# Optimization experiments

Measured on AMD Instinct MI355X. Metric: run time of the kernel, lower is better.

## Reference

```python
import jax, jax.numpy as jnp
import numpy as np

N = 100_000
E = 1_600_000
IN, HID, OUT, ED = 128, 128, 64, 16
NEG_SLOPE = 0.2  # PyG GATConv default leaky_relu slope


def segment_softmax(logits, seg, num_segments):
    m = jax.ops.segment_max(logits, seg, num_segments=num_segments)
    m = jnp.where(jnp.isfinite(m), m, 0.0)
    e = jnp.exp(logits - m[seg])
    s = jax.ops.segment_sum(e, seg, num_segments=num_segments)
    return e / (s[seg] + 1e-16)


def gat_conv(x, edge_index, W, a_src, a_dst, b, edge_attr=None, We=None, ae=None):
    """PyG GATConv, heads=1, add_self_loops=True, fill_value='mean'."""
    n = x.shape[0]
    h = x @ W  # [N, C]
    loop = jnp.arange(n, dtype=edge_index.dtype)
    src = jnp.concatenate([edge_index[0], loop])  # [E+N]
    dst = jnp.concatenate([edge_index[1], loop])
    alpha = (h * a_src).sum(-1)[src] + (h * a_dst).sum(-1)[dst]  # [E+N]
    if edge_attr is not None:
        # self-loop edge_attr filled with per-destination mean (PyG fill_value='mean')
        cnt = jax.ops.segment_sum(jnp.ones((edge_attr.shape[0],), edge_attr.dtype), edge_index[1], num_segments=n)
        mean_attr = jax.ops.segment_sum(edge_attr, edge_index[1], num_segments=n) / jnp.maximum(cnt, 1.0)[:, None]
        ea = jnp.concatenate([edge_attr, mean_attr], axis=0)  # [E+N, ED]
        alpha = alpha + (ea @ We) @ ae
    alpha = jax.nn.leaky_relu(alpha, NEG_SLOPE)
    alpha = segment_softmax(alpha, dst, n)
    out = jax.ops.segment_sum(alpha[:, None] * h[src], dst, num_segments=n)  # scatter-add
    return out + b


def setup_inputs() -> dict:
    key = jax.random.key(0)
    ks = iter(jax.random.split(key, 32))
    g = lambda shape, fan: (jax.random.normal(next(ks), shape, jnp.float32) * (1.0 / np.sqrt(fan)))
    inp = {
        "x": jax.random.normal(next(ks), (N, IN), jnp.float32),
        "edge_index": jax.random.randint(next(ks), (2, E), 0, N, jnp.int32),
        "edge_attr": jax.random.normal(next(ks), (E, ED), jnp.float32),
        # conv1 (no edge_attr)
        "W1": g((IN, HID), IN), "a1_src": g((HID,), HID), "a1_dst": g((HID,), HID), "b1": jnp.zeros((HID,), jnp.float32),
        # conv2 (with edge_attr)
        "W2": g((HID, HID), HID), "a2_src": g((HID,), HID), "a2_dst": g((HID,), HID), "b2": jnp.zeros((HID,), jnp.float32),
        "We2": g((ED, HID), ED), "ae2": g((HID,), HID),
        # initial residual linear
        "Wr": g((IN, HID), IN), "br": jnp.zeros((HID,), jnp.float32),
        # conv_mu
        "Wmu": g((HID, OUT), HID), "amu_src": g((OUT,), OUT), "amu_dst": g((OUT,), OUT), "bmu": jnp.zeros((OUT,), jnp.float32),
        "Wemu": g((ED, OUT), ED), "aemu": g((OUT,), OUT),
        # conv_logstd
        "Wls": g((HID, OUT), HID), "als_src": g((OUT,), OUT), "als_dst": g((OUT,), OUT), "bls": jnp.zeros((OUT,), jnp.float32),
        "Wels": g((ED, OUT), ED), "aels": g((OUT,), OUT),
    }
    return inp


def reference(x, edge_index, edge_attr,
              W1, a1_src, a1_dst, b1,
              W2, a2_src, a2_dst, b2, We2, ae2,
              Wr, br,
              Wmu, amu_src, amu_dst, bmu, Wemu, aemu,
              Wls, als_src, als_dst, bls, Wels, aels):
    h = jax.nn.relu(gat_conv(x, edge_index, W1, a1_src, a1_dst, b1))
    h = jax.nn.relu(gat_conv(h, edge_index, W2, a2_src, a2_dst, b2, edge_attr, We2, ae2))
    h = h + (x @ Wr + br)  # initial residual
    mu = gat_conv(h, edge_index, Wmu, amu_src, amu_dst, bmu, edge_attr, Wemu, aemu)
    logstd = gat_conv(h, edge_index, Wls, als_src, als_dst, bls, edge_attr, Wels, aels)
    return mu, logstd
```

## Files before the change

### kernel.cpp

```cpp
#include <hip/hip_runtime.h>

#define NN 100000
#define NE 1600000
#define BSH 9
#define NBUK 196
#define NPG 8

typedef __attribute__((ext_vector_type(8))) short bf16x8;
typedef __attribute__((ext_vector_type(4))) float f32x4;

__device__ __forceinline__ float grp_sum16(float v){
  #pragma unroll
  for (int o = 8; o; o >>= 1) v += __shfl_xor(v, o, 16);
  return v;
}
__device__ __forceinline__ float grp_sum32(float v){
  #pragma unroll
  for (int o = 16; o; o >>= 1) v += __shfl_xor(v, o, 32);
  return v;
}
__device__ __forceinline__ float bf2f(unsigned short x){
  return __uint_as_float(((unsigned)x) << 16);
}
__device__ __forceinline__ unsigned short f2bf(float f){
  unsigned u = __float_as_uint(f);
  return (unsigned short)((u + 0x7FFFu + ((u >> 16) & 1u)) >> 16);
}

__global__ void prep_w_kernel(const float* __restrict__ W1, const float* __restrict__ W2,
                              const float* __restrict__ Wr, const float* __restrict__ Wmu,
                              const float* __restrict__ Wls,
                              unsigned short* __restrict__ W1t, unsigned short* __restrict__ W2t,
                              unsigned short* __restrict__ Wrt, unsigned short* __restrict__ Wmlt){
  int b = blockIdx.x, t = threadIdx.x;
  for (int it = 0; it < 64; it++){
    int idx = it*256 + t;
    int k = idx >> 7, c = idx & 127;
    float v; unsigned short* dst;
    if (b == 0){ v = W1[k*128+c]; dst = W1t; }
    else if (b == 1){ v = W2[k*128+c]; dst = W2t; }
    else if (b == 2){ v = Wr[k*128+c]; dst = Wrt; }
    else { v = (c & 1) ? Wls[k*64 + (c>>1)] : Wmu[k*64 + (c>>1)]; dst = Wmlt; }
    dst[c*128 + k] = f2bf(v);
  }
}

__global__ void wvec_kernel(const float* __restrict__ We2, const float* __restrict__ ae2,
                            const float* __restrict__ Wemu, const float* __restrict__ aemu,
                            const float* __restrict__ Wels, const float* __restrict__ aels,
                            float* __restrict__ wv){
  int t = threadIdx.x;
  if (t < 16){
    float s = 0.f; for (int c = 0; c < 128; c++) s += We2[t*128+c]*ae2[c];
    wv[t] = s;
  } else if (t < 32){
    int k = t-16; float s = 0.f; for (int c = 0; c < 64; c++) s += Wemu[k*64+c]*aemu[c];
    wv[16+k] = s;
  } else if (t < 48){
    int k = t-32; float s = 0.f; for (int c = 0; c < 64; c++) s += Wels[k*64+c]*aels[c];
// ... 94 lines not shown
    hbase[t] = c ? atomicAdd(&gbfill[t], c) : 0u;
  }
  __syncthreads();
  #pragma unroll
  for (int k = 0; k < 4; k++){
    if (val[k]){
      unsigned pos = atomicAdd(&hcur[b[k]], 1);
      unsigned slot = gbbase[b[k]] + hbase[b[k]] + pos;
      bdu[slot] = make_uint2((unsigned)d[k], (unsigned)u[k]);
      bw[slot]  = w[k];
    }
  }
}

__global__ __launch_bounds__(1024) void place_kernel(const uint2* __restrict__ bdu,
                                                     const float4* __restrict__ bw,
                                                     const unsigned* __restrict__ gbbase,
                                                     int* __restrict__ rowptr,
                                                     unsigned* __restrict__ csr_u,
                                                     float* __restrict__ ewp2,
                                                     float2* __restrict__ ewpmuls){
  __shared__ unsigned h[512], incl[512], cur[512];
  int b = blockIdx.x, t = threadIdx.x;
  unsigned cbase = gbbase[b];
  unsigned cnt = gbbase[b+1] - cbase;
  if (t < 512) h[t] = 0;
  __syncthreads();
  for (unsigned i = t; i < cnt; i += 1024)
    atomicAdd(&h[bdu[cbase+i].x & 511], 1);
  __syncthreads();
  if (t < 512) incl[t] = h[t];
  __syncthreads();
  for (int o = 1; o < 512; o <<= 1){
    unsigned add = (t >= o && t < 512) ? incl[t-o] : 0;
    __syncthreads();
    if (t < 512) incl[t] += add;
    __syncthreads();
  }
  if (t < 512){
    cur[t] = 0;
    int node = (b << BSH) + t;
    if (node < NN) rowptr[node] = (int)(cbase + incl[t] - h[t]);
  }
  __syncthreads();
  for (unsigned i = t; i < cnt; i += 1024){
    uint2 du = bdu[cbase+i];
    unsigned ld = du.x & 511;
    unsigned pos = atomicAdd(&cur[ld], 1);
    unsigned slot = cbase + (incl[ld] - h[ld]) + pos;
    float4 w = bw[cbase+i];
    csr_u[slot] = du.y;
    ewp2[slot] = w.x;
    ewpmuls[slot] = make_float2(w.y, w.z);
  }
}

template<int OUT, int DOTS>
__global__ __launch_bounds__(256) void gemm_bf16(const unsigned short* __restrict__ Xb,
                                                 const unsigned short* __restrict__ Wt,
                                                 void* __restrict__ Y,
                                                 const float* __restrict__ bias, int nrows,
                                                 const float* __restrict__ va,
                                                 const float* __restrict__ vb,
                                                 const float* __restrict__ vc,
                                                 const float* __restrict__ vd,
                                                 float* __restrict__ sOut,
                                                 float* __restrict__ dOut){
  __shared__ uint4 As[128*16];
  __shared__ uint4 Bs[128*16];
  int t = threadIdx.x;
  int row0 = blockIdx.x * 128;
  #pragma unroll
  for (int p = 0; p < 8; p++){
    int idx = p*256 + t;
    int r = idx >> 4, cir = idx & 15;
    uint4 v = make_uint4(0,0,0,0);
    if (row0 + r < nrows) v = *(const uint4*)(Xb + ((size_t)(row0+r))*128 + cir*8);
    As[r*16 + (cir ^ (r & 7))] = v;
  }
  #pragma unroll
  for (int p = 0; p < 8; p++){
    int idx = p*256 + t;
    int r = idx >> 4, cir = idx & 15;
    Bs[r*16 + (cir ^ (r & 7))] = *(const uint4*)(Wt + (size_t)r*128 + cir*8);
  }
  __syncthreads();
  int w = t >> 6, l = t & 63;
  int lr = l & 15;
  int lk = l >> 4;
  const bf16x8* As8 = (const bf16x8*)As;
  const bf16x8* Bs8 = (const bf16x8*)Bs;
  f32x4 acc[2][8];
  f32x4 zero = {0.f, 0.f, 0.f, 0.f};
  #pragma unroll
  for (int m = 0; m < 2; m++)
    #pragma unroll
    for (int n = 0; n < 8; n++) acc[m][n] = zero;
  #pragma unroll
  for (int ks = 0; ks < 4; ks++){
    bf16x8 a0, a1, bf[8];
    { int r = w*32 + lr;      a0 = As8[r*16 + ((ks*4+lk) ^ (r&7))]; }
    { int r = w*32 + 16 + lr; a1 = As8[r*16 + ((ks*4+lk) ^ (r&7))]; }
    #pragma unroll
    for (int nt = 0; nt < 8; nt++){
      int r = nt*16 + lr;
      bf[nt] = Bs8[r*16 + ((ks*4+lk) ^ (r&7))];
// ... 24 lines not shown
    }
  }
  if constexpr (DOTS == 2){
    #pragma unroll
    for (int mt = 0; mt < 2; mt++){
      #pragma unroll
      for (int i = 0; i < 4; i++){
        float pmu = 0.f, pdm = 0.f, pls = 0.f, pdl = 0.f;
        #pragma unroll
        for (int nt = 0; nt < 8; nt++){
          float av = acc[mt][nt][i];
          int col = nt*16 + lr;
          int c = col >> 1;
          if (col & 1){ pls = fmaf(av, vc[c], pls); pdl = fmaf(av, vd[c], pdl); }
          else        { pmu = fmaf(av, va[c], pmu); pdm = fmaf(av, vb[c], pdm); }
        }
        pmu = grp_sum16(pmu); pdm = grp_sum16(pdm);
        pls = grp_sum16(pls); pdl = grp_sum16(pdl);
        int r = row0 + w*32 + mt*16 + lk*4 + i;
        if (lr == 0 && r < nrows){
          ((float2*)sOut)[r] = make_float2(pmu, pls);
          ((float2*)dOut)[r] = make_float2(pdm, pdl);
        }
      }
    }
  }
  #pragma unroll
  for (int mt = 0; mt < 2; mt++){
    int gr0 = row0 + w*32 + mt*16 + lk*4;
    #pragma unroll
    for (int nt = 0; nt < 8; nt++){
      int col = nt*16 + lr;
      float bv = (OUT >= 1) ? bias[col] : 0.f;
      #pragma unroll
      for (int i = 0; i < 4; i++){
        int r = gr0 + i;
        if (r < nrows){
          float o = acc[mt][nt][i] + bv;
          if constexpr (OUT == 1) ((float*)Y)[(size_t)r*128 + col] = o;
          else ((unsigned short*)Y)[(size_t)r*128 + col] = f2bf(o);
        }
      }
    }
  }
}

template<bool HAS_EW>
__global__ __launch_bounds__(256) void agg_conv(const unsigned short* __restrict__ Hb,
                                                const float* __restrict__ s,
                                                const float* __restrict__ dsc,
                                                const float* __restrict__ ewp,
                                                const int* __restrict__ rowptr,
                                                const unsigned* __restrict__ csr_u,
                                                const float* __restrict__ bias,
                                                const unsigned short* __restrict__ residb,
                                                unsigned short* __restrict__ out){
  int g = (blockIdx.x * blockDim.x + threadIdx.x) >> 5;
  int lig = threadIdx.x & 31;
  int c0 = lig*4;
  float4 bv = *(const float4*)(bias + c0);
  int v0 = g * NPG;
  int vend = v0 + NPG; if (vend > NN) vend = NN;
  for (int v = v0; v < vend; v++){
    int rs = rowptr[v], re = rowptr[v+1];
    int deg = re - rs;
    float d_v = dsc[v];
    float acc[4] = {0.f,0.f,0.f,0.f};
    float pl = 0.f, ewl = 0.f;
    for (int base = rs; base < re; base += 32){
      int i = base + lig;
      int u = 0; float w = 0.f;
      if (i < re){
        u = (int)csr_u[i];
        float e = HAS_EW ? ewp[i] : 0.f;
        if (HAS_EW) ewl += e;
        float a = s[u] + d_v + e;
        float l = a > 0.f ? a : 0.2f*a;
        w = __expf(l);
      }
      pl += w;
      int nv = re - base; if (nv > 32) nv = 32;
      for (int j = 0; j < nv; j += 8){
        uint2 q[8]; float wj[8];
        #pragma unroll
        for (int k = 0; k < 8; k++){
          int uk = __shfl(u, j+k, 32);
          wj[k] = __shfl(w, j+k, 32);
          q[k] = *(const uint2*)(Hb + (size_t)uk*128 + c0);
        }
        #pragma unroll
        for (int k = 0; k < 8; k++){
          acc[0] = fmaf(wj[k], __uint_as_float(q[k].x << 16), acc[0]);
          acc[1] = fmaf(wj[k], __uint_as_float(q[k].x & 0xFFFF0000u), acc[1]);
          acc[2] = fmaf(wj[k], __uint_as_float(q[k].y << 16), acc[2]);
          acc[3] = fmaf(wj[k], __uint_as_float(q[k].y & 0xFFFF0000u), acc[3]);
        }
      }
    }
    float p = grp_sum32(pl);
    float ews = HAS_EW ? grp_sum32(ewl) : 0.f;
    float selfa = s[v] + d_v + (HAS_EW ? ews / (float)(deg > 1 ? deg : 1) : 0.f);
    float lself = selfa > 0.f ? selfa : 0.2f*selfa;
    float wself = __expf(lself);
    p += wself;
    {
      uint2 q = *(const uint2*)(Hb + (size_t)v*128 + c0);
      acc[0] = fmaf(wself, __uint_as_float(q.x << 16), acc[0]);
      acc[1] = fmaf(wself, __uint_as_float(q.x & 0xFFFF0000u), acc[1]);
      acc[2] = fmaf(wself, __uint_as_float(q.y << 16), acc[2]);
      acc[3] = fmaf(wself, __uint_as_float(q.y & 0xFFFF0000u), acc[3]);
    }
    float inv = 1.f / p;
    float o0 = fmaxf(acc[0]*inv + bv.x, 0.f);
    float o1 = fmaxf(acc[1]*inv + bv.y, 0.f);
    float o2 = fmaxf(acc[2]*inv + bv.z, 0.f);
    float o3 = fmaxf(acc[3]*inv + bv.w, 0.f);
    if (HAS_EW){
      uint2 r = *(const uint2*)(residb + (size_t)v*128 + c0);
      o0 += __uint_as_float(r.x << 16);
      o1 += __uint_as_float(r.x & 0xFFFF0000u);
      o2 += __uint_as_float(r.y << 16);
      o3 += __uint_as_float(r.y & 0xFFFF0000u);
    }
    uint2 ow;
    ow.x = (unsigned)f2bf(o0) | ((unsigned)f2bf(o1) << 16);
    ow.y = (unsigned)f2bf(o2) | ((unsigned)f2bf(o3) << 16);
    *(uint2*)(out + (size_t)v*128 + c0) = ow;
  }
}

__global__ __launch_bounds__(256) void agg_muls(const unsigned short* __restrict__ Yb,
                                                const float2* __restrict__ sg,
                                                const float2* __restrict__ dg,
                                                const float2* __restrict__ ewpmuls,
                                                const int* __restrict__ rowptr,
                                                const unsigned* __restrict__ csr_u,
                                                const float* __restrict__ bmu,
                                                const float* __restrict__ bls,
                                                float* __restrict__ outmu,
                                                float* __restrict__ outls){
  int g = (blockIdx.x * blockDim.x + threadIdx.x) >> 5;
  int lig = threadIdx.x & 31;
  int c0 = lig*2;
  float2 bmv = make_float2(bmu[c0], bmu[c0+1]);
  float2 blv = make_float2(bls[c0], bls[c0+1]);
  int v0 = g * NPG;
  int vend = v0 + NPG; if (vend > NN) vend = NN;
  for (int v = v0; v < vend; v++){
    int rs = rowptr[v], re = rowptr[v+1];
    int deg = re - rs;
    float2 dv = dg[v];
    float accmu[2] = {0.f,0.f}, accls[2] = {0.f,0.f};
    float pmu = 0.f, pls = 0.f, ewlmu = 0.f, ewlls = 0.f;
    for (int base = rs; base < re; base += 32){
      int i = base + lig;
      int u = 0; float wmu = 0.f, wls = 0.f;
      if (i < re){
        u = (int)csr_u[i];
        float2 su = sg[u];
        float2 ee = ewpmuls[i];
        ewlmu += ee.x; ewlls += ee.y;
        float amu = su.x + dv.x + ee.x;
        float als = su.y + dv.y + ee.y;
        float lmu = amu > 0.f ? amu : 0.2f*amu;
        float lls = als > 0.f ? als : 0.2f*als;
        wmu = __expf(lmu); wls = __expf(lls);
      }
      pmu += wmu; pls += wls;
      int nv = re - base; if (nv > 32) nv = 32;
      for (int j = 0; j < nv; j += 8){
        uint2 q[8]; float wm[8], wl[8];
        #pragma unroll
        for (int k = 0; k < 8; k++){
          int uk = __shfl(u, j+k, 32);
          wm[k] = __shfl(wmu, j+k, 32);
          wl[k] = __shfl(wls, j+k, 32);
          q[k] = *(const uint2*)(Yb + (size_t)uk*128 + lig*4);
        }
        #pragma unroll
        for (int k = 0; k < 8; k++){
          accmu[0] = fmaf(wm[k], __uint_as_float(q[k].x << 16), accmu[0]);
          accls[0] = fmaf(wl[k], __uint_as_float(q[k].x & 0xFFFF0000u), accls[0]);
          accmu[1] = fmaf(wm[k], __uint_as_float(q[k].y << 16), accmu[1]);
          accls[1] = fmaf(wl[k], __uint_as_float(q[k].y & 0xFFFF0000u), accls[1]);
        }
      }
    }
    float Pmu = grp_sum32(pmu), Pls = grp_sum32(pls);
    float Emu = grp_sum32(ewlmu), Els = grp_sum32(ewlls);
    float2 sv = sg[v];
    float dnm = (float)(deg > 1 ? deg : 1);
    float selfmu = sv.x + dv.x + Emu/dnm;
    float selfls = sv.y + dv.y + Els/dnm;
    float lmu = selfmu > 0.f ? selfmu : 0.2f*selfmu;
    float lls = selfls > 0.f ? selfls : 0.2f*selfls;
    float wmu_s = __expf(lmu), wls_s = __expf(lls);
    Pmu += wmu_s; Pls += wls_s;
    {
      uint2 q = *(const uint2*)(Yb + (size_t)v*128 + lig*4);
      accmu[0] = fmaf(wmu_s, __uint_as_float(q.x << 16), accmu[0]);
      accls[0] = fmaf(wls_s, __uint_as_float(q.x & 0xFFFF0000u), accls[0]);
      accmu[1] = fmaf(wmu_s, __uint_as_float(q.y << 16), accmu[1]);
      accls[1] = fmaf(wls_s, __uint_as_float(q.y & 0xFFFF0000u), accls[1]);
    }
    float imu = 1.f/Pmu, ils = 1.f/Pls;
    float2 omu = make_float2(accmu[0]*imu + bmv.x, accmu[1]*imu + bmv.y);
    float2 ols = make_float2(accls[0]*ils + blv.x, accls[1]*ils + blv.y);
    *(float2*)(outmu + (size_t)v*64 + c0) = omu;
    *(float2*)(outls + (size_t)v*64 + c0) = ols;
  }
}

extern "C" void kernel_launch(void* const* d_in, const int* in_sizes, int n_in,
                              void* d_out, int out_size, void* d_ws, size_t ws_size,
                              hipStream_t stream){
  const float* x    = (const float*)d_in[0];
  const int*   ei   = (const int*)  d_in[1];
  const float* ea   = (const float*)d_in[2];
  const float* W1   = (const float*)d_in[3];
  const float* a1s  = (const float*)d_in[4];
  const float* a1d  = (const float*)d_in[5];
  const float* b1   = (const float*)d_in[6];
  const float* W2   = (const float*)d_in[7];
  const float* a2s  = (const float*)d_in[8];
  const float* a2d  = (const float*)d_in[9];
  const float* b2   = (const float*)d_in[10];
  const float* We2  = (const float*)d_in[11];
  const float* ae2  = (const float*)d_in[12];
  const float* Wr   = (const float*)d_in[13];
  const float* br   = (const float*)d_in[14];
  const float* Wmu  = (const float*)d_in[15];
  const float* amus = (const float*)d_in[16];
  const float* amud = (const float*)d_in[17];
  const float* bmu  = (const float*)d_in[18];
  const float* Wemu = (const float*)d_in[19];
  const float* aemu = (const float*)d_in[20];
  const float* Wls  = (const float*)d_in[21];
  const float* alss = (const float*)d_in[22];
  const float* alsd = (const float*)d_in[23];
  const float* bls  = (const float*)d_in[24];
  const float* Wels = (const float*)d_in[25];
  const float* aels = (const float*)d_in[26];

  char* base = (char*)d_ws;
  size_t off = 0;
  auto alloc = [&](size_t bytes)->char*{
    char* p = base + off;
    off = (off + bytes + 511) & ~(size_t)511;
    return p;
  };
  int*      rowptr = (int*)   alloc((size_t)(NN+1)*4);
  unsigned* gbcnt  = (unsigned*)alloc(512*4);
  unsigned* gbfill = gbcnt + 256;
  unsigned* gbbase = (unsigned*)alloc(257*4);
  uint2*    bdu    = (uint2*) alloc((size_t)NE*8);
  float4*   bw     = (float4*)alloc((size_t)NE*16);
  unsigned* csr_u  = (unsigned*)alloc((size_t)NE*4);
  float*    ewp2   = (float*) alloc((size_t)NE*4);
  float2*   ewpmls = (float2*)alloc((size_t)NE*8);
  float*    wv     = (float*) alloc(48*4);
  float*    s1     = (float*) alloc((size_t)NN*4);
  float*    d1     = (float*) alloc((size_t)NN*4);
  float2*   sg2    = (float2*)alloc((size_t)NN*8);
  float2*   dg2    = (float2*)alloc((size_t)NN*8);
  unsigned short* W1t  = (unsigned short*)alloc(128*128*2);
  unsigned short* W2t  = (unsigned short*)alloc(128*128*2);
  unsigned short* Wrt  = (unsigned short*)alloc(128*128*2);
  unsigned short* Wmlt = (unsigned short*)alloc(128*128*2);
  unsigned short* Xb   = (unsigned short*)alloc((size_t)NN*128*2);
  unsigned short* XRb  = (unsigned short*)alloc((size_t)NN*128*2);
  unsigned short* bufA = (unsigned short*)alloc((size_t)NN*128*2);
  unsigned short* bufB = (unsigned short*)alloc((size_t)NN*128*2);
  if (off > ws_size) return;

  float* outF = (float*)d_out;
  float* muO  = outF;
  float* lsO  = outF + (size_t)NN*64;

  const int HB   = (NE + 4095)/4096;
  const int AGB  = ((NN + NPG - 1)/NPG * 32 + 255)/256;
  const int GB   = (NN + 127)/128;
  const int CB   = (NN*128/8 + 255)/256;

  prep_w_kernel<<<4, 256, 0, stream>>>(W1, W2, Wr, Wmu, Wls, W1t, W2t, Wrt, Wmlt);
  wvec_kernel<<<1, 64, 0, stream>>>(We2, ae2, Wemu, aemu, Wels, aels, wv);
  cast_x_kernel<<<CB, 256, 0, stream>>>(x, Xb);
  zero_kernel<<<2, 256, 0, stream>>>((int*)gbcnt, 512);
  ehist_kernel<<<HB, 1024, 0, stream>>>(ei, gbcnt);
  bscan_kernel<<<1, 256, 0, stream>>>(gbcnt, gbbase, rowptr);
  bin_kernel<<<HB, 1024, 0, stream>>>(ei, ea, wv, gbbase, gbfill, bdu, bw);
  place_kernel<<<NBUK, 1024, 0, stream>>>(bdu, bw, gbbase, rowptr, csr_u, ewp2, ewpmls);

  gemm_bf16<0,1><<<GB, 256, 0, stream>>>(Xb, W1t, bufA, nullptr, NN,
                                         a1s, a1d, nullptr, nullptr, s1, d1);
  agg_conv<false><<<AGB, 256, 0, stream>>>(bufA, s1, d1, nullptr, rowptr, csr_u,
                                           b1, nullptr, bufB);
  gemm_bf16<0,1><<<GB, 256, 0, stream>>>(bufB, W2t, bufA, nullptr, NN,
                                         a2s, a2d, nullptr, nullptr, s1, d1);
  gemm_bf16<2,0><<<GB, 256, 0, stream>>>(Xb, Wrt, XRb, br, NN,
                                         nullptr, nullptr, nullptr, nullptr,
                                         nullptr, nullptr);
  agg_conv<true><<<AGB, 256, 0, stream>>>(bufA, s1, d1, ewp2, rowptr, csr_u,
                                          b2, XRb, bufB);
  gemm_bf16<0,2><<<GB, 256, 0, stream>>>(bufB, Wmlt, bufA, nullptr, NN,
                                         amus, amud, alss, alsd,
                                         (float*)sg2, (float*)dg2);
  agg_muls<<<AGB, 256, 0, stream>>>(bufA, sg2, dg2, ewpmls, rowptr, csr_u,
                                    bmu, bls, muO, lsO);
}
```

Measured before the change: 491.6 us.

## Use persistent work-stealing groups with atomic counter in aggregation kernels

Replaces the static assignment of 8 nodes per 32-lane group with a persistent grid of 2048 blocks. Each group atomically grabs batches of 4 nodes from a global counter until all nodes are done. The goal is to balance load across groups despite varying node degrees and to cut tail imbalance. In exchange it adds one atomic per batch, which may contend on the shared counter, and per-kernel tick counters are zeroed in the setup kernel.

```diff
diff --git a/kernel.cpp b/kernel.cpp
--- a/kernel.cpp
+++ b/kernel.cpp
@@ -4,7 +4,7 @@
 #define NE 1600000
 #define BSH 9
 #define NBUK 196
-#define NPG 8
+#define TBATCH 4
 
 typedef __attribute__((ext_vector_type(8))) short bf16x8;
 typedef __attribute__((ext_vector_type(4))) float f32x4;
@@ -337,78 +337,83 @@
                                                 const unsigned* __restrict__ csr_u,
                                                 const float* __restrict__ bias,
                                                 const unsigned short* __restrict__ residb,
-                                                unsigned short* __restrict__ out){
-  int g = (blockIdx.x * blockDim.x + threadIdx.x) >> 5;
+                                                unsigned short* __restrict__ out,
+                                                unsigned* __restrict__ ctr){
   int lig = threadIdx.x & 31;
   int c0 = lig*4;
   float4 bv = *(const float4*)(bias + c0);
-  int v0 = g * NPG;
-  int vend = v0 + NPG; if (vend > NN) vend = NN;
-  for (int v = v0; v < vend; v++){
-    int rs = rowptr[v], re = rowptr[v+1];
-    int deg = re - rs;
-    float d_v = dsc[v];
-    float acc[4] = {0.f,0.f,0.f,0.f};
-    float pl = 0.f, ewl = 0.f;
-    for (int base = rs; base < re; base += 32){
-      int i = base + lig;
-      int u = 0; float w = 0.f;
-      if (i < re){
-        u = (int)csr_u[i];
-        float e = HAS_EW ? ewp[i] : 0.f;
-        if (HAS_EW) ewl += e;
-        float a = s[u] + d_v + e;
-        float l = a > 0.f ? a : 0.2f*a;
-        w = __expf(l);
-      }
-      pl += w;
-      int nv = re - base; if (nv > 32) nv = 32;
-      for (int j = 0; j < nv; j += 8){
-        uint2 q[8]; float wj[8];
-        #pragma unroll
-        for (int k = 0; k < 8; k++){
-          int uk = __shfl(u, j+k, 32);
-          wj[k] = __shfl(w, j+k, 32);
-          q[k] = *(const uint2*)(Hb + (size_t)uk*128 + c0);
-        }
-        #pragma unroll
-        for (int k = 0; k < 8; k++){
-          acc[0] = fmaf(wj[k], __uint_as_float(q[k].x << 16), acc[0]);
-          acc[1] = fmaf(wj[k], __uint_as_float(q[k].x & 0xFFFF0000u), acc[1]);
-          acc[2] = fmaf(wj[k], __uint_as_float(q[k].y << 16), acc[2]);
-          acc[3] = fmaf(wj[k], __uint_as_float(q[k].y & 0xFFFF0000u), acc[3]);
-        }
-      }
-    }
-    float p = grp_sum32(pl);
-    float ews = HAS_EW ? grp_sum32(ewl) : 0.f;
-    float selfa = s[v] + d_v + (HAS_EW ? ews / (float)(deg > 1 ? deg : 1) : 0.f);
-    float lself = selfa > 0.f ? selfa : 0.2f*selfa;
-    float wself = __expf(lself);
-    p += wself;
-    {
-      uint2 q = *(const uint2*)(Hb + (size_t)v*128 + c0);
-      acc[0] = fmaf(wself, __uint_as_float(q.x << 16), acc[0]);
-      acc[1] = fmaf(wself, __uint_as_float(q.x & 0xFFFF0000u), acc[1]);
-      acc[2] = fmaf(wself, __uint_as_float(q.y << 16), acc[2]);
-      acc[3] = fmaf(wself, __uint_as_float(q.y & 0xFFFF0000u), acc[3]);
-    }
-    float inv = 1.f / p;
-    float o0 = fmaxf(acc[0]*inv + bv.x, 0.f);
-    float o1 = fmaxf(acc[1]*inv + bv.y, 0.f);
-    float o2 = fmaxf(acc[2]*inv + bv.z, 0.f);
-    float o3 = fmaxf(acc[3]*inv + bv.w, 0.f);
-    if (HAS_EW){
-      uint2 r = *(const uint2*)(residb + (size_t)v*128 + c0);
-      o0 += __uint_as_float(r.x << 16);
-      o1 += __uint_as_float(r.x & 0xFFFF0000u);
-      o2 += __uint_as_float(r.y << 16);
-      o3 += __uint_as_float(r.y & 0xFFFF0000u);
-    }
-    uint2 ow;
-    ow.x = (unsigned)f2bf(o0) | ((unsigned)f2bf(o1) << 16);
-    ow.y = (unsigned)f2bf(o2) | ((unsigned)f2bf(o3) << 16);
-    *(uint2*)(out + (size_t)v*128 + c0) = ow;
+  for (;;){
+    unsigned nb = 0;
+    if (lig == 0) nb = atomicAdd(ctr, TBATCH);
+    nb = __shfl((int)nb, 0, 32);
+    if (nb >= NN) break;
+    int vend = nb + TBATCH; if (vend > NN) vend = NN;
+    for (int v = (int)nb; v < vend; v++){
+      int rs = rowptr[v], re = rowptr[v+1];
+      int deg = re - rs;
+      float d_v = dsc[v];
+      float acc[4] = {0.f,0.f,0.f,0.f};
+      float pl = 0.f, ewl = 0.f;
+      for (int base = rs; base < re; base += 32){
+        int i = base + lig;
+        int u = 0; float w = 0.f;
+        if (i < re){
+          u = (int)csr_u[i];
+          float e = HAS_EW ? ewp[i] : 0.f;
+          if (HAS_EW) ewl += e;
+          float a = s[u] + d_v + e;
+          float l = a > 0.f ? a : 0.2f*a;
+          w = __expf(l);
+        }
+        pl += w;
+        int nv = re - base; if (nv > 32) nv = 32;
+        for (int j = 0; j < nv; j += 8){
+          uint2 q[8]; float wj[8];
+          #pragma unroll
+          for (int k = 0; k < 8; k++){
+            int uk = __shfl(u, j+k, 32);
+            wj[k] = __shfl(w, j+k, 32);
+            q[k] = *(const uint2*)(Hb + (size_t)uk*128 + c0);
+          }
+          #pragma unroll
+          for (int k = 0; k < 8; k++){
+            acc[0] = fmaf(wj[k], __uint_as_float(q[k].x << 16), acc[0]);
+            acc[1] = fmaf(wj[k], __uint_as_float(q[k].x & 0xFFFF0000u), acc[1]);
+            acc[2] = fmaf(wj[k], __uint_as_float(q[k].y << 16), acc[2]);
+            acc[3] = fmaf(wj[k], __uint_as_float(q[k].y & 0xFFFF0000u), acc[3]);
+          }
+        }
+      }
+      float p = grp_sum32(pl);
+      float ews = HAS_EW ? grp_sum32(ewl) : 0.f;
+      float selfa = s[v] + d_v + (HAS_EW ? ews / (float)(deg > 1 ? deg : 1) : 0.f);
+      float lself = selfa > 0.f ? selfa : 0.2f*selfa;
+      float wself = __expf(lself);
+      p += wself;
+      {
+        uint2 q = *(const uint2*)(Hb + (size_t)v*128 + c0);
+        acc[0] = fmaf(wself, __uint_as_float(q.x << 16), acc[0]);
+        acc[1] = fmaf(wself, __uint_as_float(q.x & 0xFFFF0000u), acc[1]);
+        acc[2] = fmaf(wself, __uint_as_float(q.y << 16), acc[2]);
+        acc[3] = fmaf(wself, __uint_as_float(q.y & 0xFFFF0000u), acc[3]);
+      }
+      float inv = 1.f / p;
+      float o0 = fmaxf(acc[0]*inv + bv.x, 0.f);
+      float o1 = fmaxf(acc[1]*inv + bv.y, 0.f);
+      float o2 = fmaxf(acc[2]*inv + bv.z, 0.f);
+      float o3 = fmaxf(acc[3]*inv + bv.w, 0.f);
+      if (HAS_EW){
+        uint2 r = *(const uint2*)(residb + (size_t)v*128 + c0);
+        o0 += __uint_as_float(r.x << 16);
+        o1 += __uint_as_float(r.x & 0xFFFF0000u);
+        o2 += __uint_as_float(r.y << 16);
+        o3 += __uint_as_float(r.y & 0xFFFF0000u);
+      }
+      uint2 ow;
+      ow.x = (unsigned)f2bf(o0) | ((unsigned)f2bf(o1) << 16);
+      ow.y = (unsigned)f2bf(o2) | ((unsigned)f2bf(o3) << 16);
+      *(uint2*)(out + (size_t)v*128 + c0) = ow;
+    }
   }
 }
 
@@ -421,76 +426,81 @@
                                                 const float* __restrict__ bmu,
                                                 const float* __restrict__ bls,
                                                 float* __restrict__ outmu,
-                                                float* __restrict__ outls){
-  int g = (blockIdx.x * blockDim.x + threadIdx.x) >> 5;
+                                                float* __restrict__ outls,
+                                                unsigned* __restrict__ ctr){
   int lig = threadIdx.x & 31;
   int c0 = lig*2;
   float2 bmv = make_float2(bmu[c0], bmu[c0+1]);
   float2 blv = make_float2(bls[c0], bls[c0+1]);
-  int v0 = g * NPG;
-  int vend = v0 + NPG; if (vend > NN) vend = NN;
-  for (int v = v0; v < vend; v++){
-    int rs = rowptr[v], re = rowptr[v+1];
-    int deg = re - rs;
-    float2 dv = dg[v];
-    float accmu[2] = {0.f,0.f}, accls[2] = {0.f,0.f};
-    float pmu = 0.f, pls = 0.f, ewlmu = 0.f, ewlls = 0.f;
-    for (int base = rs; base < re; base += 32){
-      int i = base + lig;
-      int u = 0; float wmu = 0.f, wls = 0.f;
-      if (i < re){
-        u = (int)csr_u[i];
-        float2 su = sg[u];
-        float2 ee = ewpmuls[i];
-        ewlmu += ee.x; ewlls += ee.y;
-        float amu = su.x + dv.x + ee.x;
-        float als = su.y + dv.y + ee.y;
-        float lmu = amu > 0.f ? amu : 0.2f*amu;
-        float lls = als > 0.f ? als : 0.2f*als;
-        wmu = __expf(lmu); wls = __expf(lls);
-      }
-      pmu += wmu; pls += wls;
-      int nv = re - base; if (nv > 32) nv = 32;
-      for (int j = 0; j < nv; j += 8){
-        uint2 q[8]; float wm[8], wl[8];
-        #pragma unroll
-        for (int k = 0; k < 8; k++){
-          int uk = __shfl(u, j+k, 32);
-          wm[k] = __shfl(wmu, j+k, 32);
-          wl[k] = __shfl(wls, j+k, 32);
-          q[k] = *(const uint2*)(Yb + (size_t)uk*128 + lig*4);
-        }
-        #pragma unroll
-        for (int k = 0; k < 8; k++){
-          accmu[0] = fmaf(wm[k], __uint_as_float(q[k].x << 16), accmu[0]);
-          accls[0] = fmaf(wl[k], __uint_as_float(q[k].x & 0xFFFF0000u), accls[0]);
-          accmu[1] = fmaf(wm[k], __uint_as_float(q[k].y << 16), accmu[1]);
-          accls[1] = fmaf(wl[k], __uint_as_float(q[k].y & 0xFFFF0000u), accls[1]);
-        }
-      }
-    }
-    float Pmu = grp_sum32(pmu), Pls = grp_sum32(pls);
-    float Emu = grp_sum32(ewlmu), Els = grp_sum32(ewlls);
-    float2 sv = sg[v];
-    float dnm = (float)(deg > 1 ? deg : 1);
-    float selfmu = sv.x + dv.x + Emu/dnm;
-    float selfls = sv.y + dv.y + Els/dnm;
-    float lmu = selfmu > 0.f ? selfmu : 0.2f*selfmu;
-    float lls = selfls > 0.f ? selfls : 0.2f*selfls;
-    float wmu_s = __expf(lmu), wls_s = __expf(lls);
-    Pmu += wmu_s; Pls += wls_s;
-    {
-      uint2 q = *(const uint2*)(Yb + (size_t)v*128 + lig*4);
-      accmu[0] = fmaf(wmu_s, __uint_as_float(q.x << 16), accmu[0]);
-      accls[0] = fmaf(wls_s, __uint_as_float(q.x & 0xFFFF0000u), accls[0]);
-      accmu[1] = fmaf(wmu_s, __uint_as_float(q.y << 16), accmu[1]);
-      accls[1] = fmaf(wls_s, __uint_as_float(q.y & 0xFFFF0000u), accls[1]);
-    }
-    float imu = 1.f/Pmu, ils = 1.f/Pls;
-    float2 omu = make_float2(accmu[0]*imu + bmv.x, accmu[1]*imu + bmv.y);
-    float2 ols = make_float2(accls[0]*ils + blv.x, accls[1]*ils + blv.y);
-    *(float2*)(outmu + (size_t)v*64 + c0) = omu;
-    *(float2*)(outls + (size_t)v*64 + c0) = ols;
+  for (;;){
+    unsigned nb = 0;
+    if (lig == 0) nb = atomicAdd(ctr, TBATCH);
+    nb = __shfl((int)nb, 0, 32);
+    if (nb >= NN) break;
+    int vend = nb + TBATCH; if (vend > NN) vend = NN;
+    for (int v = (int)nb; v < vend; v++){
+      int rs = rowptr[v], re = rowptr[v+1];
+      int deg = re - rs;
+      float2 dv = dg[v];
+      float accmu[2] = {0.f,0.f}, accls[2] = {0.f,0.f};
+      float pmu = 0.f, pls = 0.f, ewlmu = 0.f, ewlls = 0.f;
+      for (int base = rs; base < re; base += 32){
+        int i = base + lig;
+        int u = 0; float wmu = 0.f, wls = 0.f;
+        if (i < re){
+          u = (int)csr_u[i];
+          float2 su = sg[u];
+          float2 ee = ewpmuls[i];
+          ewlmu += ee.x; ewlls += ee.y;
+          float amu = su.x + dv.x + ee.x;
+          float als = su.y + dv.y + ee.y;
+          float lmu = amu > 0.f ? amu : 0.2f*amu;
+          float lls = als > 0.f ? als : 0.2f*als;
+          wmu = __expf(lmu); wls = __expf(lls);
+        }
+        pmu += wmu; pls += wls;
+        int nv = re - base; if (nv > 32) nv = 32;
+        for (int j = 0; j < nv; j += 8){
+          uint2 q[8]; float wm[8], wl[8];
+          #pragma unroll
+          for (int k = 0; k < 8; k++){
+            int uk = __shfl(u, j+k, 32);
+            wm[k] = __shfl(wmu, j+k, 32);
+            wl[k] = __shfl(wls, j+k, 32);
+            q[k] = *(const uint2*)(Yb + (size_t)uk*128 + lig*4);
+          }
+          #pragma unroll
+          for (int k = 0; k < 8; k++){
+            accmu[0] = fmaf(wm[k], __uint_as_float(q[k].x << 16), accmu[0]);
+            accls[0] = fmaf(wl[k], __uint_as_float(q[k].x & 0xFFFF0000u), accls[0]);
+            accmu[1] = fmaf(wm[k], __uint_as_float(q[k].y << 16), accmu[1]);
+            accls[1] = fmaf(wl[k], __uint_as_float(q[k].y & 0xFFFF0000u), accls[1]);
+          }
+        }
+      }
+      float Pmu = grp_sum32(pmu), Pls = grp_sum32(pls);
+      float Emu = grp_sum32(ewlmu), Els = grp_sum32(ewlls);
+      float2 sv = sg[v];
+      float dnm = (float)(deg > 1 ? deg : 1);
+      float selfmu = sv.x + dv.x + Emu/dnm;
+      float selfls = sv.y + dv.y + Els/dnm;
+      float lmu = selfmu > 0.f ? selfmu : 0.2f*selfmu;
+      float lls = selfls > 0.f ? selfls : 0.2f*selfls;
+      float wmu_s = __expf(lmu), wls_s = __expf(lls);
+      Pmu += wmu_s; Pls += wls_s;
+      {
+        uint2 q = *(const uint2*)(Yb + (size_t)v*128 + lig*4);
+        accmu[0] = fmaf(wmu_s, __uint_as_float(q.x << 16), accmu[0]);
+        accls[0] = fmaf(wls_s, __uint_as_float(q.x & 0xFFFF0000u), accls[0]);
+        accmu[1] = fmaf(wmu_s, __uint_as_float(q.y << 16), accmu[1]);
+        accls[1] = fmaf(wls_s, __uint_as_float(q.y & 0xFFFF0000u), accls[1]);
+      }
+      float imu = 1.f/Pmu, ils = 1.f/Pls;
+      float2 omu = make_float2(accmu[0]*imu + bmv.x, accmu[1]*imu + bmv.y);
+      float2 ols = make_float2(accls[0]*ils + blv.x, accls[1]*ils + blv.y);
+      *(float2*)(outmu + (size_t)v*64 + c0) = omu;
+      *(float2*)(outls + (size_t)v*64 + c0) = ols;
+    }
   }
 }
 
@@ -533,8 +543,9 @@
     return p;
   };
   int*      rowptr = (int*)   alloc((size_t)(NN+1)*4);
-  unsigned* gbcnt  = (unsigned*)alloc(512*4);
+  unsigned* gbcnt  = (unsigned*)alloc(520*4);
   unsigned* gbfill = gbcnt + 256;
+  unsigned* tick   = gbcnt + 512;
   unsigned* gbbase = (unsigned*)alloc(257*4);
   uint2*    bdu    = (uint2*) alloc((size_t)NE*8);
   float4*   bw     = (float4*)alloc((size_t)NE*16);
@@ -561,14 +572,14 @@
   float* lsO  = outF + (size_t)NN*64;
 
   const int HB   = (NE + 4095)/4096;
-  const int AGB  = ((NN + NPG - 1)/NPG * 32 + 255)/256;
+  const int PGB  = 2048;
   const int GB   = (NN + 127)/128;
   const int CB   = (NN*128/8 + 255)/256;
 
   prep_w_kernel<<<4, 256, 0, stream>>>(W1, W2, Wr, Wmu, Wls, W1t, W2t, Wrt, Wmlt);
   wvec_kernel<<<1, 64, 0, stream>>>(We2, ae2, Wemu, aemu, Wels, aels, wv);
   cast_x_kernel<<<CB, 256, 0, stream>>>(x, Xb);
-  zero_kernel<<<2, 256, 0, stream>>>((int*)gbcnt, 512);
+  zero_kernel<<<3, 256, 0, stream>>>((int*)gbcnt, 520);
   ehist_kernel<<<HB, 1024, 0, stream>>>(ei, gbcnt);
   bscan_kernel<<<1, 256, 0, stream>>>(gbcnt, gbbase, rowptr);
   bin_kernel<<<HB, 1024, 0, stream>>>(ei, ea, wv, gbbase, gbfill, bdu, bw);
@@ -576,18 +587,18 @@
 
   gemm_bf16<0,1><<<GB, 256, 0, stream>>>(Xb, W1t, bufA, nullptr, NN,
                                          a1s, a1d, nullptr, nullptr, s1, d1);
-  agg_conv<false><<<AGB, 256, 0, stream>>>(bufA, s1, d1, nullptr, rowptr, csr_u,
-                                           b1, nullptr, bufB);
+  agg_conv<false><<<PGB, 256, 0, stream>>>(bufA, s1, d1, nullptr, rowptr, csr_u,
+                                           b1, nullptr, bufB, tick+0);
   gemm_bf16<0,1><<<GB, 256, 0, stream>>>(bufB, W2t, bufA, nullptr, NN,
                                          a2s, a2d, nullptr, nullptr, s1, d1);
   gemm_bf16<2,0><<<GB, 256, 0, stream>>>(Xb, Wrt, XRb, br, NN,
                                          nullptr, nullptr, nullptr, nullptr,
                                          nullptr, nullptr);
-  agg_conv<true><<<AGB, 256, 0, stream>>>(bufA, s1, d1, ewp2, rowptr, csr_u,
-                                          b2, XRb, bufB);
+  agg_conv<true><<<PGB, 256, 0, stream>>>(bufA, s1, d1, ewp2, rowptr, csr_u,
+                                          b2, XRb, bufB, tick+1);
   gemm_bf16<0,2><<<GB, 256, 0, stream>>>(bufB, Wmlt, bufA, nullptr, NN,
                                          amus, amud, alss, alsd,
                                          (float*)sg2, (float*)dg2);
-  agg_muls<<<AGB, 256, 0, stream>>>(bufA, sg2, dg2, ewpmls, rowptr, csr_u,
-                                    bmu, bls, muO, lsO);
-}
+  agg_muls<<<PGB, 256, 0, stream>>>(bufA, sg2, dg2, ewpmls, rowptr, csr_u,
+                                    bmu, bls, muO, lsO, tick+2);
+}
```

Result: slower. 1.050 ms (+113.7%).

## Sort nodes by in-degree and assign one half-wave per node in aggregation

Applied to the files above, without the earlier changes.

Adds a degree histogram, scan and scatter that build a permutation of nodes grouped by in-degree. The three aggregation kernels now map each 32-lane group to one node taken from that permutation, instead of each group looping over 8 consecutive nodes. This aims to even out work within a wavefront and raise the number of groups in flight, reducing divergence and tail imbalance from varied degrees. The cost is three extra small kernels, and output writes and neighbor reads become scattered in node order, which may reduce locality.

```diff
diff --git a/kernel.cpp b/kernel.cpp
--- a/kernel.cpp
+++ b/kernel.cpp
@@ -4,7 +4,8 @@
 #define NE 1600000
 #define BSH 9
 #define NBUK 196
-#define NPG 8
+#define NDB 64
+#define NB  ((NN + 255)/256)
 
 typedef __attribute__((ext_vector_type(8))) short bf16x8;
 typedef __attribute__((ext_vector_type(4))) float f32x4;
@@ -205,6 +206,57 @@
     csr_u[slot] = du.y;
     ewp2[slot] = w.x;
     ewpmuls[slot] = make_float2(w.y, w.z);
+  }
+}
+
+__global__ void dhist_kernel(const int* __restrict__ rowptr, unsigned* __restrict__ dcnt){
+  __shared__ unsigned h[NDB];
+  int t = threadIdx.x;
+  if (t < NDB) h[t] = 0;
+  __syncthreads();
+  int v = blockIdx.x*256 + t;
+  if (v < NN){
+    int d = rowptr[v+1] - rowptr[v]; if (d > NDB-1) d = NDB-1;
+    atomicAdd(&h[d], 1);
+  }
+  __syncthreads();
+  if (t < NDB && h[t]) atomicAdd(&dcnt[t], h[t]);
+}
+
+__global__ void dscan_kernel(const unsigned* __restrict__ dcnt, unsigned* __restrict__ dbase){
+  __shared__ unsigned sh[NDB];
+  int t = threadIdx.x;
+  unsigned v = dcnt[t];
+  sh[t] = v; __syncthreads();
+  for (int o = 1; o < NDB; o <<= 1){
+    unsigned add = (t >= o) ? sh[t-o] : 0;
+    __syncthreads();
+    sh[t] += add;
+    __syncthreads();
+  }
+  dbase[t] = sh[t] - v;
+}
+
+__global__ void dscatter_kernel(const int* __restrict__ rowptr, const unsigned* __restrict__ dbase,
+                                unsigned* __restrict__ dfill, int* __restrict__ perm){
+  __shared__ unsigned hc[NDB], hb[NDB], cur[NDB];
+  int t = threadIdx.x;
+  if (t < NDB){ hc[t] = 0; cur[t] = 0; }
+  __syncthreads();
+  int v = blockIdx.x*256 + t; int d = -1;
+  if (v < NN){
+    d = rowptr[v+1] - rowptr[v]; if (d > NDB-1) d = NDB-1;
+    atomicAdd(&hc[d], 1);
+  }
+  __syncthreads();
+  if (t < NDB){
+    unsigned c = hc[t];
+    hb[t] = c ? atomicAdd(&dfill[t], c) : 0u;
+  }
+  __syncthreads();
+  if (v < NN){
+    unsigned pos = atomicAdd(&cur[d], 1);
+    perm[dbase[d] + hb[d] + pos] = v;
   }
 }
 
@@ -335,81 +387,80 @@
                                                 const float* __restrict__ ewp,
                                                 const int* __restrict__ rowptr,
                                                 const unsigned* __restrict__ csr_u,
+                                                const int* __restrict__ perm,
                                                 const float* __restrict__ bias,
                                                 const unsigned short* __restrict__ residb,
                                                 unsigned short* __restrict__ out){
   int g = (blockIdx.x * blockDim.x + threadIdx.x) >> 5;
   int lig = threadIdx.x & 31;
+  if (g >= NN) return;
+  int v = perm[g];
+  int rs = rowptr[v], re = rowptr[v+1];
+  int deg = re - rs;
+  float d_v = dsc[v];
   int c0 = lig*4;
   float4 bv = *(const float4*)(bias + c0);
-  int v0 = g * NPG;
-  int vend = v0 + NPG; if (vend > NN) vend = NN;
-  for (int v = v0; v < vend; v++){
-    int rs = rowptr[v], re = rowptr[v+1];
-    int deg = re - rs;
-    float d_v = dsc[v];
-    float acc[4] = {0.f,0.f,0.f,0.f};
-    float pl = 0.f, ewl = 0.f;
-    for (int base = rs; base < re; base += 32){
-      int i = base + lig;
-      int u = 0; float w = 0.f;
-      if (i < re){
-        u = (int)csr_u[i];
-        float e = HAS_EW ? ewp[i] : 0.f;
-        if (HAS_EW) ewl += e;
-        float a = s[u] + d_v + e;
-        float l = a > 0.f ? a : 0.2f*a;
-        w = __expf(l);
-      }
-      pl += w;
-      int nv = re - base; if (nv > 32) nv = 32;
-      for (int j = 0; j < nv; j += 8){
-        uint2 q[8]; float wj[8];
-        #pragma unroll
-        for (int k = 0; k < 8; k++){
-          int uk = __shfl(u, j+k, 32);
-          wj[k] = __shfl(w, j+k, 32);
-          q[k] = *(const uint2*)(Hb + (size_t)uk*128 + c0);
-        }
-        #pragma unroll
-        for (int k = 0; k < 8; k++){
-          acc[0] = fmaf(wj[k], __uint_as_float(q[k].x << 16), acc[0]);
-          acc[1] = fmaf(wj[k], __uint_as_float(q[k].x & 0xFFFF0000u), acc[1]);
-          acc[2] = fmaf(wj[k], __uint_as_float(q[k].y << 16), acc[2]);
-          acc[3] = fmaf(wj[k], __uint_as_float(q[k].y & 0xFFFF0000u), acc[3]);
-        }
-      }
-    }
-    float p = grp_sum32(pl);
-    float ews = HAS_EW ? grp_sum32(ewl) : 0.f;
-    float selfa = s[v] + d_v + (HAS_EW ? ews / (float)(deg > 1 ? deg : 1) : 0.f);
-    float lself = selfa > 0.f ? selfa : 0.2f*selfa;
-    float wself = __expf(lself);
-    p += wself;
-    {
-      uint2 q = *(const uint2*)(Hb + (size_t)v*128 + c0);
-      acc[0] = fmaf(wself, __uint_as_float(q.x << 16), acc[0]);
-      acc[1] = fmaf(wself, __uint_as_float(q.x & 0xFFFF0000u), acc[1]);
-      acc[2] = fmaf(wself, __uint_as_float(q.y << 16), acc[2]);
-      acc[3] = fmaf(wself, __uint_as_float(q.y & 0xFFFF0000u), acc[3]);
-    }
-    float inv = 1.f / p;
-    float o0 = fmaxf(acc[0]*inv + bv.x, 0.f);
-    float o1 = fmaxf(acc[1]*inv + bv.y, 0.f);
-    float o2 = fmaxf(acc[2]*inv + bv.z, 0.f);
-    float o3 = fmaxf(acc[3]*inv + bv.w, 0.f);
-    if (HAS_EW){
-      uint2 r = *(const uint2*)(residb + (size_t)v*128 + c0);
-      o0 += __uint_as_float(r.x << 16);
-      o1 += __uint_as_float(r.x & 0xFFFF0000u);
-      o2 += __uint_as_float(r.y << 16);
-      o3 += __uint_as_float(r.y & 0xFFFF0000u);
-    }
-    uint2 ow;
-    ow.x = (unsigned)f2bf(o0) | ((unsigned)f2bf(o1) << 16);
-    ow.y = (unsigned)f2bf(o2) | ((unsigned)f2bf(o3) << 16);
-    *(uint2*)(out + (size_t)v*128 + c0) = ow;
-  }
+  float acc[4] = {0.f,0.f,0.f,0.f};
+  float pl = 0.f, ewl = 0.f;
+  for (int base = rs; base < re; base += 32){
+    int i = base + lig;
+    int u = 0; float w = 0.f;
+    if (i < re){
+      u = (int)csr_u[i];
+      float e = HAS_EW ? ewp[i] : 0.f;
+      if (HAS_EW) ewl += e;
+      float a = s[u] + d_v + e;
+      float l = a > 0.f ? a : 0.2f*a;
+      w = __expf(l);
+    }
+    pl += w;
+    int nv = re - base; if (nv > 32) nv = 32;
+    for (int j = 0; j < nv; j += 8){
+      uint2 q[8]; float wj[8];
+      #pragma unroll
+      for (int k = 0; k < 8; k++){
+        int uk = __shfl(u, j+k, 32);
+        wj[k] = __shfl(w, j+k, 32);
+        q[k] = *(const uint2*)(Hb + (size_t)uk*128 + c0);
+      }
+      #pragma unroll
+      for (int k = 0; k < 8; k++){
+        acc[0] = fmaf(wj[k], __uint_as_float(q[k].x << 16), acc[0]);
+        acc[1] = fmaf(wj[k], __uint_as_float(q[k].x & 0xFFFF0000u), acc[1]);
+        acc[2] = fmaf(wj[k], __uint_as_float(q[k].y << 16), acc[2]);
+        acc[3] = fmaf(wj[k], __uint_as_float(q[k].y & 0xFFFF0000u), acc[3]);
+      }
+    }
+  }
+  float p = grp_sum32(pl);
+  float ews = HAS_EW ? grp_sum32(ewl) : 0.f;
+  float selfa = s[v] + d_v + (HAS_EW ? ews / (float)(deg > 1 ? deg : 1) : 0.f);
+  float lself = selfa > 0.f ? selfa : 0.2f*selfa;
+  float wself = __expf(lself);
+  p += wself;
+  {
+    uint2 q = *(const uint2*)(Hb + (size_t)v*128 + c0);
+    acc[0] = fmaf(wself, __uint_as_float(q.x << 16), acc[0]);
+    acc[1] = fmaf(wself, __uint_as_float(q.x & 0xFFFF0000u), acc[1]);
+    acc[2] = fmaf(wself, __uint_as_float(q.y << 16), acc[2]);
+    acc[3] = fmaf(wself, __uint_as_float(q.y & 0xFFFF0000u), acc[3]);
+  }
+  float inv = 1.f / p;
+  float o0 = fmaxf(acc[0]*inv + bv.x, 0.f);
+  float o1 = fmaxf(acc[1]*inv + bv.y, 0.f);
+  float o2 = fmaxf(acc[2]*inv + bv.z, 0.f);
+  float o3 = fmaxf(acc[3]*inv + bv.w, 0.f);
+  if (HAS_EW){
+    uint2 r = *(const uint2*)(residb + (size_t)v*128 + c0);
+    o0 += __uint_as_float(r.x << 16);
+    o1 += __uint_as_float(r.x & 0xFFFF0000u);
+    o2 += __uint_as_float(r.y << 16);
+    o3 += __uint_as_float(r.y & 0xFFFF0000u);
+  }
+  uint2 ow;
+  ow.x = (unsigned)f2bf(o0) | ((unsigned)f2bf(o1) << 16);
+  ow.y = (unsigned)f2bf(o2) | ((unsigned)f2bf(o3) << 16);
+  *(uint2*)(out + (size_t)v*128 + c0) = ow;
 }
 
 __global__ __launch_bounds__(256) void agg_muls(const unsigned short* __restrict__ Yb,
@@ -418,80 +469,79 @@
                                                 const float2* __restrict__ ewpmuls,
                                                 const int* __restrict__ rowptr,
                                                 const unsigned* __restrict__ csr_u,
+                                                const int* __restrict__ perm,
                                                 const float* __restrict__ bmu,
                                                 const float* __restrict__ bls,
                                                 float* __restrict__ outmu,
                                                 float* __restrict__ outls){
   int g = (blockIdx.x * blockDim.x + threadIdx.x) >> 5;
   int lig = threadIdx.x & 31;
+  if (g >= NN) return;
+  int v = perm[g];
+  int rs = rowptr[v], re = rowptr[v+1];
+  int deg = re - rs;
+  float2 dv = dg[v];
   int c0 = lig*2;
   float2 bmv = make_float2(bmu[c0], bmu[c0+1]);
   float2 blv = make_float2(bls[c0], bls[c0+1]);
-  int v0 = g * NPG;
-  int vend = v0 + NPG; if (vend > NN) vend = NN;
-  for (int v = v0; v < vend; v++){
-    int rs = rowptr[v], re = rowptr[v+1];
-    int deg = re - rs;
-    float2 dv = dg[v];
-    float accmu[2] = {0.f,0.f}, accls[2] = {0.f,0.f};
-    float pmu = 0.f, pls = 0.f, ewlmu = 0.f, ewlls = 0.f;
-    for (int base = rs; base < re; base += 32){
-      int i = base + lig;
-      int u = 0; float wmu = 0.f, wls = 0.f;
-      if (i < re){
-        u = (int)csr_u[i];
-        float2 su = sg[u];
-        float2 ee = ewpmuls[i];
-        ewlmu += ee.x; ewlls += ee.y;
-        float amu = su.x + dv.x + ee.x;
-        float als = su.y + dv.y + ee.y;
-        float lmu = amu > 0.f ? amu : 0.2f*amu;
-        float lls = als > 0.f ? als : 0.2f*als;
-        wmu = __expf(lmu); wls = __expf(lls);
-      }
-      pmu += wmu; pls += wls;
-      int nv = re - base; if (nv > 32) nv = 32;
-      for (int j = 0; j < nv; j += 8){
-        uint2 q[8]; float wm[8], wl[8];
-        #pragma unroll
-        for (int k = 0; k < 8; k++){
-          int uk = __shfl(u, j+k, 32);
-          wm[k] = __shfl(wmu, j+k, 32);
-          wl[k] = __shfl(wls, j+k, 32);
-          q[k] = *(const uint2*)(Yb + (size_t)uk*128 + lig*4);
-        }
-        #pragma unroll
-        for (int k = 0; k < 8; k++){
-          accmu[0] = fmaf(wm[k], __uint_as_float(q[k].x << 16), accmu[0]);
-          accls[0] = fmaf(wl[k], __uint_as_float(q[k].x & 0xFFFF0000u), accls[0]);
-          accmu[1] = fmaf(wm[k], __uint_as_float(q[k].y << 16), accmu[1]);
-          accls[1] = fmaf(wl[k], __uint_as_float(q[k].y & 0xFFFF0000u), accls[1]);
-        }
-      }
-    }
-    float Pmu = grp_sum32(pmu), Pls = grp_sum32(pls);
-    float Emu = grp_sum32(ewlmu), Els = grp_sum32(ewlls);
-    float2 sv = sg[v];
-    float dnm = (float)(deg > 1 ? deg : 1);
-    float selfmu = sv.x + dv.x + Emu/dnm;
-    float selfls = sv.y + dv.y + Els/dnm;
-    float lmu = selfmu > 0.f ? selfmu : 0.2f*selfmu;
-    float lls = selfls > 0.f ? selfls : 0.2f*selfls;
-    float wmu_s = __expf(lmu), wls_s = __expf(lls);
-    Pmu += wmu_s; Pls += wls_s;
-    {
-      uint2 q = *(const uint2*)(Yb + (size_t)v*128 + lig*4);
-      accmu[0] = fmaf(wmu_s, __uint_as_float(q.x << 16), accmu[0]);
-      accls[0] = fmaf(wls_s, __uint_as_float(q.x & 0xFFFF0000u), accls[0]);
-      accmu[1] = fmaf(wmu_s, __uint_as_float(q.y << 16), accmu[1]);
-      accls[1] = fmaf(wls_s, __uint_as_float(q.y & 0xFFFF0000u), accls[1]);
-    }
-    float imu = 1.f/Pmu, ils = 1.f/Pls;
-    float2 omu = make_float2(accmu[0]*imu + bmv.x, accmu[1]*imu + bmv.y);
-    float2 ols = make_float2(accls[0]*ils + blv.x, accls[1]*ils + blv.y);
-    *(float2*)(outmu + (size_t)v*64 + c0) = omu;
-    *(float2*)(outls + (size_t)v*64 + c0) = ols;
-  }
+  float accmu[2] = {0.f,0.f}, accls[2] = {0.f,0.f};
+  float pmu = 0.f, pls = 0.f, ewlmu = 0.f, ewlls = 0.f;
+  for (int base = rs; base < re; base += 32){
+    int i = base + lig;
+    int u = 0; float wmu = 0.f, wls = 0.f;
+    if (i < re){
+      u = (int)csr_u[i];
+      float2 su = sg[u];
+      float2 ee = ewpmuls[i];
+      ewlmu += ee.x; ewlls += ee.y;
+      float amu = su.x + dv.x + ee.x;
+      float als = su.y + dv.y + ee.y;
+      float lmu = amu > 0.f ? amu : 0.2f*amu;
+      float lls = als > 0.f ? als : 0.2f*als;
+      wmu = __expf(lmu); wls = __expf(lls);
+    }
+    pmu += wmu; pls += wls;
+    int nv = re - base; if (nv > 32) nv = 32;
+    for (int j = 0; j < nv; j += 8){
+      uint2 q[8]; float wm[8], wl[8];
+      #pragma unroll
+      for (int k = 0; k < 8; k++){
+        int uk = __shfl(u, j+k, 32);
+        wm[k] = __shfl(wmu, j+k, 32);
+        wl[k] = __shfl(wls, j+k, 32);
+        q[k] = *(const uint2*)(Yb + (size_t)uk*128 + lig*4);
+      }
+      #pragma unroll
+      for (int k = 0; k < 8; k++){
+        accmu[0] = fmaf(wm[k], __uint_as_float(q[k].x << 16), accmu[0]);
+        accls[0] = fmaf(wl[k], __uint_as_float(q[k].x & 0xFFFF0000u), accls[0]);
+        accmu[1] = fmaf(wm[k], __uint_as_float(q[k].y << 16), accmu[1]);
+        accls[1] = fmaf(wl[k], __uint_as_float(q[k].y & 0xFFFF0000u), accls[1]);
+      }
+    }
+  }
+  float Pmu = grp_sum32(pmu), Pls = grp_sum32(pls);
+  float Emu = grp_sum32(ewlmu), Els = grp_sum32(ewlls);
+  float2 sv = sg[v];
+  float dnm = (float)(deg > 1 ? deg : 1);
+  float selfmu = sv.x + dv.x + Emu/dnm;
+  float selfls = sv.y + dv.y + Els/dnm;
+  float lmu = selfmu > 0.f ? selfmu : 0.2f*selfmu;
+  float lls = selfls > 0.f ? selfls : 0.2f*selfls;
+  float wmu_s = __expf(lmu), wls_s = __expf(lls);
+  Pmu += wmu_s; Pls += wls_s;
+  {
+    uint2 q = *(const uint2*)(Yb + (size_t)v*128 + lig*4);
+    accmu[0] = fmaf(wmu_s, __uint_as_float(q.x << 16), accmu[0]);
+    accls[0] = fmaf(wls_s, __uint_as_float(q.x & 0xFFFF0000u), accls[0]);
+    accmu[1] = fmaf(wmu_s, __uint_as_float(q.y << 16), accmu[1]);
+    accls[1] = fmaf(wls_s, __uint_as_float(q.y & 0xFFFF0000u), accls[1]);
+  }
+  float imu = 1.f/Pmu, ils = 1.f/Pls;
+  float2 omu = make_float2(accmu[0]*imu + bmv.x, accmu[1]*imu + bmv.y);
+  float2 ols = make_float2(accls[0]*ils + blv.x, accls[1]*ils + blv.y);
+  *(float2*)(outmu + (size_t)v*64 + c0) = omu;
+  *(float2*)(outls + (size_t)v*64 + c0) = ols;
 }
 
 extern "C" void kernel_launch(void* const* d_in, const int* in_sizes, int n_in,
@@ -533,9 +583,13 @@
     return p;
   };
   int*      rowptr = (int*)   alloc((size_t)(NN+1)*4);
-  unsigned* gbcnt  = (unsigned*)alloc(512*4);
+  unsigned* gbcnt  = (unsigned*)alloc(640*4);
   unsigned* gbfill = gbcnt + 256;
+  unsigned* dcnt   = gbcnt + 512;
+  unsigned* dfill  = gbcnt + 576;
   unsigned* gbbase = (unsigned*)alloc(257*4);
+  unsigned* dbase  = (unsigned*)alloc(64*4);
+  int*      perm   = (int*)   alloc((size_t)NN*4);
   uint2*    bdu    = (uint2*) alloc((size_t)NE*8);
   float4*   bw     = (float4*)alloc((size_t)NE*16);
   unsigned* csr_u  = (unsigned*)alloc((size_t)NE*4);
@@ -561,33 +615,36 @@
   float* lsO  = outF + (size_t)NN*64;
 
   const int HB   = (NE + 4095)/4096;
-  const int AGB  = ((NN + NPG - 1)/NPG * 32 + 255)/256;
+  const int WB32 = (NN*32 + 255)/256;
   const int GB   = (NN + 127)/128;
   const int CB   = (NN*128/8 + 255)/256;
 
   prep_w_kernel<<<4, 256, 0, stream>>>(W1, W2, Wr, Wmu, Wls, W1t, W2t, Wrt, Wmlt);
   wvec_kernel<<<1, 64, 0, stream>>>(We2, ae2, Wemu, aemu, Wels, aels, wv);
   cast_x_kernel<<<CB, 256, 0, stream>>>(x, Xb);
-  zero_kernel<<<2, 256, 0, stream>>>((int*)gbcnt, 512);
+  zero_kernel<<<3, 256, 0, stream>>>((int*)gbcnt, 640);
   ehist_kernel<<<HB, 1024, 0, stream>>>(ei, gbcnt);
   bscan_kernel<<<1, 256, 0, stream>>>(gbcnt, gbbase, rowptr);
   bin_kernel<<<HB, 1024, 0, stream>>>(ei, ea, wv, gbbase, gbfill, bdu, bw);
   place_kernel<<<NBUK, 1024, 0, stream>>>(bdu, bw, gbbase, rowptr, csr_u, ewp2, ewpmls);
+  dhist_kernel<<<NB, 256, 0, stream>>>(rowptr, dcnt);
+  dscan_kernel<<<1, 64, 0, stream>>>(dcnt, dbase);
+  dscatter_kernel<<<NB, 256, 0, stream>>>(rowptr, dbase, dfill, perm);
 
   gemm_bf16<0,1><<<GB, 256, 0, stream>>>(Xb, W1t, bufA, nullptr, NN,
                                          a1s, a1d, nullptr, nullptr, s1, d1);
-  agg_conv<false><<<AGB, 256, 0, stream>>>(bufA, s1, d1, nullptr, rowptr, csr_u,
-                                           b1, nullptr, bufB);
+  agg_conv<false><<<WB32, 256, 0, stream>>>(bufA, s1, d1, nullptr, rowptr, csr_u,
+                                            perm, b1, nullptr, bufB);
   gemm_bf16<0,1><<<GB, 256, 0, stream>>>(bufB, W2t, bufA, nullptr, NN,
                                          a2s, a2d, nullptr, nullptr, s1, d1);
   gemm_bf16<2,0><<<GB, 256, 0, stream>>>(Xb, Wrt, XRb, br, NN,
                                          nullptr, nullptr, nullptr, nullptr,
                                          nullptr, nullptr);
-  agg_conv<true><<<AGB, 256, 0, stream>>>(bufA, s1, d1, ewp2, rowptr, csr_u,
-                                          b2, XRb, bufB);
+  agg_conv<true><<<WB32, 256, 0, stream>>>(bufA, s1, d1, ewp2, rowptr, csr_u,
+                                           perm, b2, XRb, bufB);
   gemm_bf16<0,2><<<GB, 256, 0, stream>>>(bufB, Wmlt, bufA, nullptr, NN,
                                          amus, amud, alss, alsd,
                                          (float*)sg2, (float*)dg2);
-  agg_muls<<<AGB, 256, 0, stream>>>(bufA, sg2, dg2, ewpmls, rowptr, csr_u,
-                                    bmu, bls, muO, lsO);
-}
+  agg_muls<<<WB32, 256, 0, stream>>>(bufA, sg2, dg2, ewpmls, rowptr, csr_u,
+                                     perm, bmu, bls, muO, lsO);
+}
```

Result: faster. 480.4 us (-2.3%).
